# Performance work log

Hardware: AMD Instinct MI355X
Metric: run time of the kernel (lower is better)

## Reference

```python
import jax, jax.numpy as jnp
import numpy as np

B, S, D = 8, 2048, 512
MINF = 20000.0  # matches tf code's -20000.0 mask constant


def setup_inputs() -> dict:
    key = jax.random.key(0)
    k1, k2, k3 = jax.random.split(key, 3)
    x1 = jax.random.normal(k1, (B, S, D), dtype=jnp.float32)
    x2 = jax.random.normal(k2, (B, S, D), dtype=jnp.float32)
    # glorot_normal init for the learned (S, S) positional kernel
    std = np.sqrt(2.0 / (S + S)).astype(np.float32)
    kernel = jax.random.normal(k3, (S, S), dtype=jnp.float32) * std
    return {"x1": x1, "x2": x2, "kernel": kernel}


def reference(x1, x2, kernel):
    S_ = kernel.shape[0]
    # tf.matmul(kernel, inputs[i]) broadcasts (S,S) @ (B,S,D) -> (B,S,D)
    h1 = jnp.einsum('st,btd->bsd', kernel, x1)
    h2 = jnp.einsum('st,btd->bsd', kernel, x2)
    # att_scores: (B, S, S)
    scores = jnp.einsum('bsd,btd->bst', h1, h2)
    d_k = jnp.asarray(S_, dtype=scores.dtype) ** 0.5
    # upper_m[i,j] = -20000 for j > i (strictly upper), else 0; added BEFORE scaling
    row = jnp.arange(S_)
    mask = jnp.where(row[None, :] > row[:, None], -MINF, 0.0).astype(scores.dtype)
    attn = jax.nn.softmax((scores + mask) / d_k, axis=-1)
    # note: output attends over h1 (not h2), as in the original code
    return jnp.einsum('bst,btd->bsd', attn, h1)
```

## Files before the change

kernel.cpp:

```cpp
#include <hip/hip_runtime.h>
#include <hip/hip_bf16.h>

#define S_DIM 2048
#define D_DIM 512
#define B_DIM 8
#define SCALE 0.02209708691207961f

typedef __hip_bfloat16 bf16;
typedef short bf16x8 __attribute__((ext_vector_type(8)));
typedef float f32x4 __attribute__((ext_vector_type(4)));

__device__ __forceinline__ unsigned short f2b(float f) {
  __hip_bfloat16 h = __float2bfloat16(f);
  return __builtin_bit_cast(unsigned short, h);
}

__device__ __forceinline__ void load_lds16(const void* g, void* l) {
  __builtin_amdgcn_global_load_lds((const __attribute__((address_space(1))) void*)g,
                                   (__attribute__((address_space(3))) void*)l, 16, 0, 0);
}

__global__ void convert_k(const float* __restrict__ in, bf16* __restrict__ out, int n8) {
  int i = blockIdx.x * blockDim.x + threadIdx.x;
  if (i >= n8) return;
  const float4* p = (const float4*)in;
  float4 a = p[2 * i], b = p[2 * i + 1];
  bf16x8 r;
  r[0] = f2b(a.x); r[1] = f2b(a.y); r[2] = f2b(a.z); r[3] = f2b(a.w);
  r[4] = f2b(b.x); r[5] = f2b(b.y); r[6] = f2b(b.z); r[7] = f2b(b.w);
  ((bf16x8*)out)[i] = r;
}

__global__ void transpose_f2b(const float* __restrict__ in, bf16* __restrict__ out) {
  __shared__ float tile[32][33];
  int b = blockIdx.z;
  int c0 = blockIdx.x * 32;
  int r0 = blockIdx.y * 32;
  const float* ib = in + (size_t)b * S_DIM * D_DIM;
  bf16* ob = out + (size_t)b * S_DIM * D_DIM;
  int lr = threadIdx.x >> 5, lc = threadIdx.x & 31;
#pragma unroll
  for (int i = 0; i < 4; i++)
    tile[lr + i * 8][lc] = ib[(size_t)(r0 + lr + i * 8) * D_DIM + c0 + lc];
  __syncthreads();
#pragma unroll
  for (int i = 0; i < 4; i++) {
    int cc = lr + i * 8;
    ob[(size_t)(c0 + cc) * S_DIM + r0 + lc] = __float2bfloat16(tile[lc][cc]);
  }
}

__global__ void transpose_b2b(const bf16* __restrict__ in, bf16* __restrict__ out) {
  __shared__ bf16 tile[32][33];
  int b = blockIdx.z;
  int c0 = blockIdx.x * 32;
  int r0 = blockIdx.y * 32;
  const bf16* ib = in + (size_t)b * S_DIM * D_DIM;
  bf16* ob = out + (size_t)b * S_DIM * D_DIM;
  int lr = threadIdx.x >> 5, lc = threadIdx.x & 31;
#pragma unroll
  for (int i = 0; i < 4; i++)
    tile[lr + i * 8][lc] = ib[(size_t)(r0 + lr + i * 8) * D_DIM + c0 + lc];
  __syncthreads();
#pragma unroll
  for (int i = 0; i < 4; i++) {
    int cc = lr + i * 8;
    ob[(size_t)(c0 + cc) * S_DIM + r0 + lc] = tile[lc][cc];
  }
}

__global__ __launch_bounds__(256, 2) void gemm_bt(
    const bf16* __restrict__ A,
    const bf16* __restrict__ B1, const bf16* __restrict__ B2,
    bf16* __restrict__ C1, bf16* __restrict__ C2) {
  const int N = D_DIM, K = S_DIM;
  __shared__ bf16 As[128][32];
  __shared__ bf16 Bs[128][32];
  int z = blockIdx.z;
  int b = z & 7, which = z >> 3;
  const bf16* Bb = (which ? B2 : B1) + (size_t)b * D_DIM * S_DIM;
  bf16* Cb = (which ? C2 : C1) + (size_t)b * S_DIM * D_DIM;
  int m0 = blockIdx.y * 128, n0 = blockIdx.x * 128;
  int tid = threadIdx.x, wave = tid >> 6, lane = tid & 63;
  int wr = wave >> 1, wc = wave & 1;
  int srow = lane >> 2;
  int skh = (lane & 3) * 8;
  int lr16 = lane & 15, lk = (lane >> 4) * 8;
  f32x4 acc[4][4];
#pragma unroll
  for (int m = 0; m < 4; m++)
#pragma unroll
    for (int n = 0; n < 4; n++) acc[m][n] = (f32x4){0, 0, 0, 0};

  for (int k0 = 0; k0 < K; k0 += 32) {
#pragma unroll
    for (int c = 0; c < 2; c++) {
      int chunk = wave * 2 + c;
      int row = chunk * 16 + srow;
      load_lds16(A + (size_t)(m0 + row) * K + k0 + skh, (char*)&As[0][0] + chunk * 1024);
      load_lds16(Bb + (size_t)(n0 + row) * K + k0 + skh, (char*)&Bs[0][0] + chunk * 1024);
    }
    __syncthreads();
    bf16x8 af[4], bfr[4];
#pragma unroll
    for (int m = 0; m < 4; m++) af[m] = *(const bf16x8*)&As[wr * 64 + m * 16 + lr16][lk];
#pragma unroll
    for (int n = 0; n < 4; n++) bfr[n] = *(const bf16x8*)&Bs[wc * 64 + n * 16 + lr16][lk];
#pragma unroll
    for (int m = 0; m < 4; m++)
#pragma unroll
      for (int n = 0; n < 4; n++)
        acc[m][n] = __builtin_amdgcn_mfma_f32_16x16x32_bf16(af[m], bfr[n], acc[m][n], 0, 0, 0);
    __syncthreads();
  }
#pragma unroll
  for (int m = 0; m < 4; m++) {
    int grow0 = m0 + wr * 64 + m * 16 + (lane >> 4) * 4;
#pragma unroll
    for (int n = 0; n < 4; n++) {
      int gcol = n0 + wc * 64 + n * 16 + lr16;
#pragma unroll
      for (int r = 0; r < 4; r++)
        Cb[(size_t)(grow0 + r) * N + gcol] = __float2bfloat16(acc[m][n][r]);
    }
  }
}

__global__ __launch_bounds__(256, 2) void gemm_score(
    const bf16* __restrict__ H1, const bf16* __restrict__ H2,
    bf16* __restrict__ E, float* __restrict__ rowsum) {
  const int K = D_DIM;
  __shared__ bf16 As[128][32];
  __shared__ bf16 Bs[128][32];
  int pid = blockIdx.x;
  int b = pid & 7, tri = pid >> 3;
  int mt = (int)((sqrtf(8.0f * (float)tri + 1.0f) - 1.0f) * 0.5f);
  while ((mt + 1) * (mt + 2) / 2 <= tri) mt++;
  while (mt * (mt + 1) / 2 > tri) mt--;
  int nt = tri - mt * (mt + 1) / 2;
  const bf16* Ab = H1 + (size_t)b * S_DIM * D_DIM;
  const bf16* Bb = H2 + (size_t)b * S_DIM * D_DIM;
  bf16* Eb = E + (size_t)b * S_DIM * S_DIM;
  float* rs = rowsum + b * S_DIM;
  int m0 = mt * 128, n0 = nt * 128;
  int tid = threadIdx.x, wave = tid >> 6, lane = tid & 63;
  int wr = wave >> 1, wc = wave & 1;
  int srow = lane >> 2;
  int skh = (lane & 3) * 8;
  int l15 = lane & 15, lhi = lane >> 4;
  int lk = lhi * 8;
  f32x4 acc[4][4];
#pragma unroll
  for (int m = 0; m < 4; m++)
#pragma unroll
    for (int n = 0; n < 4; n++) acc[m][n] = (f32x4){0, 0, 0, 0};

  for (int k0 = 0; k0 < K; k0 += 32) {
#pragma unroll
    for (int c = 0; c < 2; c++) {
      int chunk = wave * 2 + c;
      int row = chunk * 16 + srow;
      load_lds16(Ab + (size_t)(m0 + row) * K + k0 + skh, (char*)&As[0][0] + chunk * 1024);
      load_lds16(Bb + (size_t)(n0 + row) * K + k0 + skh, (char*)&Bs[0][0] + chunk * 1024);
    }
    __syncthreads();
    bf16x8 af[4], bfr[4];
#pragma unroll
    for (int m = 0; m < 4; m++) af[m] = *(const bf16x8*)&As[wr * 64 + m * 16 + l15][lk];
#pragma unroll
    for (int n = 0; n < 4; n++) bfr[n] = *(const bf16x8*)&Bs[wc * 64 + n * 16 + l15][lk];
#pragma unroll
    for (int m = 0; m < 4; m++)
#pragma unroll
      for (int n = 0; n < 4; n++)
        acc[m][n] = __builtin_amdgcn_mfma_f32_16x16x32_bf16(af[m], bfr[n], acc[m][n], 0, 0, 0);
    __syncthreads();
  }
  float rp[4][4];
#pragma unroll
  for (int m = 0; m < 4; m++)
#pragma unroll
    for (int r = 0; r < 4; r++) rp[m][r] = 0.0f;
#pragma unroll
  for (int m = 0; m < 4; m++) {
#pragma unroll
    for (int n = 0; n < 4; n++) {
      int tg = n0 + wc * 64 + n * 16 + l15;
#pragma unroll
      for (int r = 0; r < 4; r++) {
        int sg = m0 + wr * 64 + m * 16 + lhi * 4 + r;
        float v = 0.0f;
        if (tg <= sg) v = __expf(acc[m][n][r] * SCALE);
        bf16 bv = __float2bfloat16(v);
        Eb[(size_t)sg * S_DIM + tg] = bv;
        rp[m][r] += __bfloat162float(bv);
      }
    }
  }
#pragma unroll
  for (int m = 0; m < 4; m++) {
#pragma unroll
    for (int r = 0; r < 4; r++) {
      float v = rp[m][r];
#pragma unroll
      for (int off = 1; off < 16; off <<= 1) v += __shfl_xor(v, off);
      if (l15 == 0) {
        int sg = m0 + wr * 64 + m * 16 + lhi * 4 + r;
        atomicAdd(rs + sg, v);
      }
    }
  }
}

__global__ __launch_bounds__(256, 2) void gemm_pv(
    const bf16* __restrict__ E, const bf16* __restrict__ H1T,
    const float* __restrict__ rowsum, float* __restrict__ out) {
  __shared__ bf16 As[128][32];
  __shared__ bf16 Bs[128][32];
  int pid = blockIdx.x;
  int b = pid & 7;
  int r_ = pid >> 3;
  int nt = r_ & 3;
  int mb = r_ >> 2;
  int mt = (mb < 8) ? 2 * mb : 31 - 2 * mb;
  int m0 = mt * 128, n0 = nt * 128;
  int KMAX = (mt + 1) * 128;
  const bf16* Ab = E + (size_t)b * S_DIM * S_DIM;
  const bf16* Bb = H1T + (size_t)b * D_DIM * S_DIM;
  const float* rs = rowsum + b * S_DIM;
  float* Cb = out + (size_t)b * S_DIM * D_DIM;
  int tid = threadIdx.x, wave = tid >> 6, lane = tid & 63;
  int wr = wave >> 1, wc = wave & 1;
  int srow = lane >> 2;
  int skh = (lane & 3) * 8;
  int l15 = lane & 15, lhi = lane >> 4;
  int lk = lhi * 8;
  f32x4 acc[4][4];
#pragma unroll
  for (int m = 0; m < 4; m++)
#pragma unroll
    for (int n = 0; n < 4; n++) acc[m][n] = (f32x4){0, 0, 0, 0};

  for (int k0 = 0; k0 < KMAX; k0 += 32) {
#pragma unroll
    for (int c = 0; c < 2; c++) {
      int chunk = wave * 2 + c;
      int row = chunk * 16 + srow;
      load_lds16(Ab + (size_t)(m0 + row) * S_DIM + k0 + skh, (char*)&As[0][0] + chunk * 1024);
      load_lds16(Bb + (size_t)(n0 + row) * S_DIM + k0 + skh, (char*)&Bs[0][0] + chunk * 1024);
    }
    __syncthreads();
    bf16x8 af[4], bfr[4];
#pragma unroll
    for (int m = 0; m < 4; m++) af[m] = *(const bf16x8*)&As[wr * 64 + m * 16 + l15][lk];
#pragma unroll
    for (int n = 0; n < 4; n++) bfr[n] = *(const bf16x8*)&Bs[wc * 64 + n * 16 + l15][lk];
#pragma unroll
    for (int m = 0; m < 4; m++)
#pragma unroll
      for (int n = 0; n < 4; n++)
        acc[m][n] = __builtin_amdgcn_mfma_f32_16x16x32_bf16(af[m], bfr[n], acc[m][n], 0, 0, 0);
    __syncthreads();
  }
#pragma unroll
  for (int m = 0; m < 4; m++) {
#pragma unroll
    for (int r = 0; r < 4; r++) {
      int sg = m0 + wr * 64 + m * 16 + lhi * 4 + r;
      float inv = 1.0f / rs[sg];
#pragma unroll
      for (int n = 0; n < 4; n++) {
        int gcol = n0 + wc * 64 + n * 16 + l15;
        Cb[(size_t)sg * D_DIM + gcol] = acc[m][n][r] * inv;
      }
    }
  }
}

extern "C" void kernel_launch(void* const* d_in, const int* in_sizes, int n_in,
                              void* d_out, int out_size, void* d_ws, size_t ws_size,
                              hipStream_t stream) {
  const float* x1 = (const float*)d_in[0];
  const float* x2 = (const float*)d_in[1];
  const float* km = (const float*)d_in[2];
  float* out = (float*)d_out;
  char* ws = (char*)d_ws;
  bf16* E    = (bf16*)(ws);
  bf16* Kbf  = (bf16*)(ws);
  bf16* x1t  = (bf16*)(ws + (8ull << 20));
  bf16* x2t  = (bf16*)(ws + (24ull << 20));
  bf16* h1n  = (bf16*)(ws + (64ull << 20));
  bf16* h2n  = (bf16*)(ws + (80ull << 20));
  bf16* h1t  = (bf16*)(ws + (96ull << 20));
  float* rowsum = (float*)(ws + (112ull << 20));

  convert_k<<<2048, 256, 0, stream>>>(km, Kbf, (S_DIM * S_DIM) / 8);
  transpose_f2b<<<dim3(16, 64, 8), 256, 0, stream>>>(x1, x1t);
  transpose_f2b<<<dim3(16, 64, 8), 256, 0, stream>>>(x2, x2t);
  gemm_bt<<<dim3(4, 16, 16), 256, 0, stream>>>(Kbf, x1t, x2t, h1n, h2n);
  transpose_b2b<<<dim3(16, 64, 8), 256, 0, stream>>>(h1n, h1t);
  hipMemsetAsync(rowsum, 0, B_DIM * S_DIM * sizeof(float), stream);
  gemm_score<<<136 * 8, 256, 0, stream>>>(h1n, h2n, E, rowsum);
  gemm_pv<<<512, 256, 0, stream>>>(E, h1t, rowsum, out);
}
```

Baseline: 197.2 us.

## Replace projection GEMM with triple-buffered, swizzled 256x128 tile kernel

Replaces the simple single-buffered gemm_bt projection GEMM with gemm_h. It uses 512-thread blocks on 256x128 output tiles and a K step of 64. A three-stage ring of LDS buffers is filled by asynchronous global-to-LDS loads, throttled with explicit vmcnt waits, so global loads overlap MFMA work. XOR-swizzled LDS addressing avoids bank conflicts, and s_setprio is raised around the MFMA burst. The x1/x2 work items are addressed as one contiguous 16-item batch through adjacent workspace regions. The cost is 144 KB of dynamic LDS per block, which limits occupancy, and the code depends on that exact workspace layout.

```diff
diff --git a/kernel.cpp b/kernel.cpp
--- a/kernel.cpp
+++ b/kernel.cpp
@@ -69,59 +69,109 @@
   }
 }
 
-__global__ __launch_bounds__(256, 2) void gemm_bt(
-    const bf16* __restrict__ A,
-    const bf16* __restrict__ B1, const bf16* __restrict__ B2,
-    bf16* __restrict__ C1, bf16* __restrict__ C2) {
-  const int N = D_DIM, K = S_DIM;
-  __shared__ bf16 As[128][32];
-  __shared__ bf16 Bs[128][32];
-  int z = blockIdx.z;
-  int b = z & 7, which = z >> 3;
-  const bf16* Bb = (which ? B2 : B1) + (size_t)b * D_DIM * S_DIM;
-  bf16* Cb = (which ? C2 : C1) + (size_t)b * S_DIM * D_DIM;
-  int m0 = blockIdx.y * 128, n0 = blockIdx.x * 128;
-  int tid = threadIdx.x, wave = tid >> 6, lane = tid & 63;
-  int wr = wave >> 1, wc = wave & 1;
-  int srow = lane >> 2;
-  int skh = (lane & 3) * 8;
-  int lr16 = lane & 15, lk = (lane >> 4) * 8;
+__global__ __launch_bounds__(512, 2) void gemm_h(
+    const bf16* __restrict__ A, const bf16* __restrict__ X, bf16* __restrict__ H) {
+  extern __shared__ char smem[];
+  const int pid = blockIdx.x;
+  const int item = pid & 15;
+  const int tt = pid >> 4;
+  const int mt = tt >> 2, ntl = tt & 3;
+  const int m0 = mt * 256, n0 = ntl * 128;
+  const bf16* Xi = X + (size_t)item * (D_DIM * S_DIM);
+  bf16* Hi = H + (size_t)item * (S_DIM * D_DIM);
+
+  const int tid = threadIdx.x;
+  const int w = tid >> 6, L = tid & 63;
+  const int l15 = L & 15, lhi = L >> 4;
+  const int wr = w >> 1, wc = w & 1;
+  const int lr8 = L >> 3;
+  const int sslot = ((L & 7) ^ lr8) * 8;
+
+  const bf16* paA[4];
+  const bf16* paB[2];
+#pragma unroll
+  for (int ld = 0; ld < 4; ld++)
+    paA[ld] = A + (size_t)(m0 + 32 * w + 8 * ld + lr8) * 2048 + sslot;
+#pragma unroll
+  for (int ld = 0; ld < 2; ld++)
+    paB[ld] = Xi + (size_t)(n0 + 16 * w + 8 * ld + lr8) * 2048 + sslot;
+
+  char* rA0 = smem;
+  char* rA1 = smem + 32768;
+  char* rA2 = smem + 65536;
+  char* rB0 = smem + 98304;
+  char* rB1 = smem + 98304 + 16384;
+  char* rB2 = smem + 98304 + 32768;
+
+  auto stage = [&](int t2, char* dA, char* dB) {
+#pragma unroll
+    for (int ld = 0; ld < 4; ld++)
+      load_lds16(paA[ld] + t2 * 64, dA + ((w * 4 + ld) << 10));
+#pragma unroll
+    for (int ld = 0; ld < 2; ld++)
+      load_lds16(paB[ld] + t2 * 64, dB + ((w * 2 + ld) << 10));
+  };
+
+  int offA[2][4], offB[2][4];
+#pragma unroll
+  for (int kk = 0; kk < 2; kk++) {
+#pragma unroll
+    for (int m = 0; m < 4; m++)
+      offA[kk][m] = (wr * 64 + m * 16 + l15) * 128 + ((((kk << 2) + lhi) ^ (L & 7)) << 4);
+#pragma unroll
+    for (int n = 0; n < 4; n++)
+      offB[kk][n] = (wc * 64 + n * 16 + l15) * 128 + ((((kk << 2) + lhi) ^ (L & 7)) << 4);
+  }
+
   f32x4 acc[4][4];
 #pragma unroll
   for (int m = 0; m < 4; m++)
 #pragma unroll
     for (int n = 0; n < 4; n++) acc[m][n] = (f32x4){0, 0, 0, 0};
 
-  for (int k0 = 0; k0 < K; k0 += 32) {
-#pragma unroll
-    for (int c = 0; c < 2; c++) {
-      int chunk = wave * 2 + c;
-      int row = chunk * 16 + srow;
-      load_lds16(A + (size_t)(m0 + row) * K + k0 + skh, (char*)&As[0][0] + chunk * 1024);
-      load_lds16(Bb + (size_t)(n0 + row) * K + k0 + skh, (char*)&Bs[0][0] + chunk * 1024);
-    }
-    __syncthreads();
-    bf16x8 af[4], bfr[4];
-#pragma unroll
-    for (int m = 0; m < 4; m++) af[m] = *(const bf16x8*)&As[wr * 64 + m * 16 + lr16][lk];
-#pragma unroll
-    for (int n = 0; n < 4; n++) bfr[n] = *(const bf16x8*)&Bs[wc * 64 + n * 16 + lr16][lk];
-#pragma unroll
-    for (int m = 0; m < 4; m++)
-#pragma unroll
-      for (int n = 0; n < 4; n++)
-        acc[m][n] = __builtin_amdgcn_mfma_f32_16x16x32_bf16(af[m], bfr[n], acc[m][n], 0, 0, 0);
-    __syncthreads();
-  }
+  stage(0, rA0, rB0);
+  stage(1, rA1, rB1);
+
+#pragma unroll 1
+  for (int t = 0; t < 32; ++t) {
+    if (t < 31) asm volatile("s_waitcnt vmcnt(6)" ::: "memory");
+    else        asm volatile("s_waitcnt vmcnt(0)" ::: "memory");
+    __builtin_amdgcn_s_barrier();
+    asm volatile("" ::: "memory");
+    if (t < 30) stage(t + 2, rA2, rB2);
+
+    bf16x8 af[2][4], bfr[2][4];
+#pragma unroll
+    for (int kk = 0; kk < 2; kk++) {
+#pragma unroll
+      for (int m = 0; m < 4; m++) af[kk][m] = *(const bf16x8*)(rA0 + offA[kk][m]);
+#pragma unroll
+      for (int n = 0; n < 4; n++) bfr[kk][n] = *(const bf16x8*)(rB0 + offB[kk][n]);
+    }
+    __builtin_amdgcn_s_setprio(1);
+#pragma unroll
+    for (int kk = 0; kk < 2; kk++)
+#pragma unroll
+      for (int m = 0; m < 4; m++)
+#pragma unroll
+        for (int n = 0; n < 4; n++)
+          acc[m][n] = __builtin_amdgcn_mfma_f32_16x16x32_bf16(af[kk][m], bfr[kk][n], acc[m][n], 0, 0, 0);
+    __builtin_amdgcn_s_setprio(0);
+
+    char* tA = rA0; rA0 = rA1; rA1 = rA2; rA2 = tA;
+    char* tB = rB0; rB0 = rB1; rB1 = rB2; rB2 = tB;
+  }
+
 #pragma unroll
   for (int m = 0; m < 4; m++) {
-    int grow0 = m0 + wr * 64 + m * 16 + (lane >> 4) * 4;
 #pragma unroll
     for (int n = 0; n < 4; n++) {
-      int gcol = n0 + wc * 64 + n * 16 + lr16;
-#pragma unroll
-      for (int r = 0; r < 4; r++)
-        Cb[(size_t)(grow0 + r) * N + gcol] = __float2bfloat16(acc[m][n][r]);
+      int col = n0 + wc * 64 + n * 16 + l15;
+#pragma unroll
+      for (int r = 0; r < 4; r++) {
+        int row = m0 + wr * 64 + m * 16 + lhi * 4 + r;
+        Hi[(size_t)row * D_DIM + col] = __float2bfloat16(acc[m][n][r]);
+      }
     }
   }
 }
@@ -288,16 +338,15 @@
   bf16* E    = (bf16*)(ws);
   bf16* Kbf  = (bf16*)(ws);
   bf16* x1t  = (bf16*)(ws + (8ull << 20));
-  bf16* x2t  = (bf16*)(ws + (24ull << 20));
   bf16* h1n  = (bf16*)(ws + (64ull << 20));
-  bf16* h2n  = (bf16*)(ws + (80ull << 20));
   bf16* h1t  = (bf16*)(ws + (96ull << 20));
   float* rowsum = (float*)(ws + (112ull << 20));
+  bf16* h2n  = (bf16*)(ws + (80ull << 20));
 
   convert_k<<<2048, 256, 0, stream>>>(km, Kbf, (S_DIM * S_DIM) / 8);
   transpose_f2b<<<dim3(16, 64, 8), 256, 0, stream>>>(x1, x1t);
-  transpose_f2b<<<dim3(16, 64, 8), 256, 0, stream>>>(x2, x2t);
-  gemm_bt<<<dim3(4, 16, 16), 256, 0, stream>>>(Kbf, x1t, x2t, h1n, h2n);
+  transpose_f2b<<<dim3(16, 64, 8), 256, 0, stream>>>(x2, (bf16*)(ws + (24ull << 20)));
+  gemm_h<<<512, 512, 147456, stream>>>(Kbf, x1t, h1n);
   transpose_b2b<<<dim3(16, 64, 8), 256, 0, stream>>>(h1n, h1t);
   hipMemsetAsync(rowsum, 0, B_DIM * S_DIM * sizeof(float), stream);
   gemm_score<<<136 * 8, 256, 0, stream>>>(h1n, h2n, E, rowsum);
```

After: 190.5 us. -3.4%, faster.

## Use 256x256 tiles with triple-buffered LDS pipeline for projection and score GEMMs

Applied to the files above, without the earlier changes.

Replaces the 128x128 projection and score GEMMs with 512-thread kernels computing 256x256 tiles. They stage operands through a three-buffer LDS ring with XOR-swizzled slots, using explicit vmcnt waits and one barrier per k-step. MFMA operands are swapped so each lane holds four consecutive output columns, which allows packed 8-byte bf16 stores. The score kernel applies the causal mask only on diagonal tiles and reduces row sums with two shuffles. The projection kernel covers both inputs in one flattened grid. The cost is 96KB of dynamic LDS per block, fewer blocks overall, and more wasted work in the now-larger diagonal tiles.

```diff
diff --git a/kernel.cpp b/kernel.cpp
--- a/kernel.cpp
+++ b/kernel.cpp
@@ -13,6 +13,9 @@
 __device__ __forceinline__ unsigned short f2b(float f) {
   __hip_bfloat16 h = __float2bfloat16(f);
   return __builtin_bit_cast(unsigned short, h);
+}
+__device__ __forceinline__ float b2f(unsigned short s) {
+  return __bfloat162float(__builtin_bit_cast(__hip_bfloat16, s));
 }
 
 __device__ __forceinline__ void load_lds16(const void* g, void* l) {
@@ -69,146 +72,208 @@
   }
 }
 
-__global__ __launch_bounds__(256, 2) void gemm_bt(
-    const bf16* __restrict__ A,
-    const bf16* __restrict__ B1, const bf16* __restrict__ B2,
-    bf16* __restrict__ C1, bf16* __restrict__ C2) {
-  const int N = D_DIM, K = S_DIM;
-  __shared__ bf16 As[128][32];
-  __shared__ bf16 Bs[128][32];
-  int z = blockIdx.z;
-  int b = z & 7, which = z >> 3;
-  const bf16* Bb = (which ? B2 : B1) + (size_t)b * D_DIM * S_DIM;
-  bf16* Cb = (which ? C2 : C1) + (size_t)b * S_DIM * D_DIM;
-  int m0 = blockIdx.y * 128, n0 = blockIdx.x * 128;
-  int tid = threadIdx.x, wave = tid >> 6, lane = tid & 63;
-  int wr = wave >> 1, wc = wave & 1;
-  int srow = lane >> 2;
-  int skh = (lane & 3) * 8;
-  int lr16 = lane & 15, lk = (lane >> 4) * 8;
-  f32x4 acc[4][4];
-#pragma unroll
-  for (int m = 0; m < 4; m++)
+__global__ __launch_bounds__(512, 2) void gemm_h(
+    const bf16* __restrict__ A, const bf16* __restrict__ X, bf16* __restrict__ H) {
+  extern __shared__ char smem[];
+  const int pid = blockIdx.x;
+  const int mt = pid & 7;
+  const int r_ = pid >> 3;
+  const int ntile = r_ & 1;
+  const int item = r_ >> 1;
+  const int m0 = mt * 256, n0 = ntile * 256;
+  const bf16* Xi = X + (size_t)item * (D_DIM * S_DIM);
+  bf16* Hi = H + (size_t)item * (S_DIM * D_DIM);
+
+  const int tid = threadIdx.x;
+  const int w = tid >> 6, L = tid & 63;
+  const int l15 = L & 15, lhi = L >> 4;
+  const int wr = w >> 2, wn = w & 3;
+
+  const int srow = tid >> 2;
+  const int sslot = ((tid & 3) ^ ((tid >> 3) & 3)) * 8;
+  const bf16* pA[2];
+  const bf16* pB[2];
+#pragma unroll
+  for (int ld = 0; ld < 2; ld++) {
+    pA[ld] = A + (size_t)(m0 + ld * 128 + srow) * 2048 + sslot;
+    pB[ld] = Xi + (size_t)(n0 + ld * 128 + srow) * 2048 + sslot;
+  }
+
+  char* A0 = smem;          char* A1 = smem + 16384;  char* A2 = smem + 32768;
+  char* B0 = smem + 49152;  char* B1 = smem + 65536;  char* B2 = smem + 81920;
+
+  auto stage = [&](int t2, char* dA, char* dB) {
+#pragma unroll
+    for (int ld = 0; ld < 2; ld++)
+      load_lds16(pA[ld] + t2 * 32, dA + ld * 8192 + w * 1024);
+#pragma unroll
+    for (int ld = 0; ld < 2; ld++)
+      load_lds16(pB[ld] + t2 * 32, dB + ld * 8192 + w * 1024);
+  };
+
+  const int xo = (lhi ^ ((l15 >> 1) & 3)) << 4;
+  int offA[8], offB[4];
+#pragma unroll
+  for (int m = 0; m < 8; m++) offA[m] = (wr * 128 + m * 16 + l15) * 64 + xo;
+#pragma unroll
+  for (int n = 0; n < 4; n++) offB[n] = (wn * 64 + n * 16 + l15) * 64 + xo;
+
+  f32x4 acc[8][4];
+#pragma unroll
+  for (int m = 0; m < 8; m++)
 #pragma unroll
     for (int n = 0; n < 4; n++) acc[m][n] = (f32x4){0, 0, 0, 0};
 
-  for (int k0 = 0; k0 < K; k0 += 32) {
-#pragma unroll
-    for (int c = 0; c < 2; c++) {
-      int chunk = wave * 2 + c;
-      int row = chunk * 16 + srow;
-      load_lds16(A + (size_t)(m0 + row) * K + k0 + skh, (char*)&As[0][0] + chunk * 1024);
-      load_lds16(Bb + (size_t)(n0 + row) * K + k0 + skh, (char*)&Bs[0][0] + chunk * 1024);
+  stage(0, A0, B0);
+  stage(1, A1, B1);
+
+#pragma unroll 1
+  for (int t = 0; t < 64; ++t) {
+    if (t < 63) asm volatile("s_waitcnt vmcnt(4)" ::: "memory");
+    else        asm volatile("s_waitcnt vmcnt(0)" ::: "memory");
+    __builtin_amdgcn_s_barrier();
+    asm volatile("" ::: "memory");
+    if (t < 62) stage(t + 2, A2, B2);
+
+    bf16x8 af[8], bfv[4];
+#pragma unroll
+    for (int m = 0; m < 8; m++) af[m] = *(const bf16x8*)(A0 + offA[m]);
+#pragma unroll
+    for (int n = 0; n < 4; n++) bfv[n] = *(const bf16x8*)(B0 + offB[n]);
+    __builtin_amdgcn_s_setprio(1);
+#pragma unroll
+    for (int m = 0; m < 8; m++)
+#pragma unroll
+      for (int n = 0; n < 4; n++)
+        acc[m][n] = __builtin_amdgcn_mfma_f32_16x16x32_bf16(bfv[n], af[m], acc[m][n], 0, 0, 0);
+    __builtin_amdgcn_s_setprio(0);
+
+    char* tA = A0; A0 = A1; A1 = A2; A2 = tA;
+    char* tB = B0; B0 = B1; B1 = B2; B2 = tB;
+  }
+
+#pragma unroll
+  for (int m = 0; m < 8; m++) {
+    int grow = m0 + wr * 128 + m * 16 + l15;
+#pragma unroll
+    for (int n = 0; n < 4; n++) {
+      int gcol = n0 + wn * 64 + n * 16 + lhi * 4;
+      uint2 u;
+      u.x = ((unsigned)f2b(acc[m][n][1]) << 16) | f2b(acc[m][n][0]);
+      u.y = ((unsigned)f2b(acc[m][n][3]) << 16) | f2b(acc[m][n][2]);
+      *(uint2*)(Hi + (size_t)grow * D_DIM + gcol) = u;
     }
-    __syncthreads();
-    bf16x8 af[4], bfr[4];
-#pragma unroll
-    for (int m = 0; m < 4; m++) af[m] = *(const bf16x8*)&As[wr * 64 + m * 16 + lr16][lk];
-#pragma unroll
-    for (int n = 0; n < 4; n++) bfr[n] = *(const bf16x8*)&Bs[wc * 64 + n * 16 + lr16][lk];
-#pragma unroll
-    for (int m = 0; m < 4; m++)
-#pragma unroll
-      for (int n = 0; n < 4; n++)
-        acc[m][n] = __builtin_amdgcn_mfma_f32_16x16x32_bf16(af[m], bfr[n], acc[m][n], 0, 0, 0);
-    __syncthreads();
-  }
-#pragma unroll
-  for (int m = 0; m < 4; m++) {
-    int grow0 = m0 + wr * 64 + m * 16 + (lane >> 4) * 4;
-#pragma unroll
-    for (int n = 0; n < 4; n++) {
-      int gcol = n0 + wc * 64 + n * 16 + lr16;
-#pragma unroll
-      for (int r = 0; r < 4; r++)
-        Cb[(size_t)(grow0 + r) * N + gcol] = __float2bfloat16(acc[m][n][r]);
-    }
-  }
-}
-
-__global__ __launch_bounds__(256, 2) void gemm_score(
+  }
+}
+
+__global__ __launch_bounds__(512, 2) void gemm_score(
     const bf16* __restrict__ H1, const bf16* __restrict__ H2,
     bf16* __restrict__ E, float* __restrict__ rowsum) {
-  const int K = D_DIM;
-  __shared__ bf16 As[128][32];
-  __shared__ bf16 Bs[128][32];
-  int pid = blockIdx.x;
-  int b = pid & 7, tri = pid >> 3;
+  extern __shared__ char smem[];
+  const int pid = blockIdx.x;
+  const int b = pid & 7;
+  const int tri = pid >> 3;
   int mt = (int)((sqrtf(8.0f * (float)tri + 1.0f) - 1.0f) * 0.5f);
   while ((mt + 1) * (mt + 2) / 2 <= tri) mt++;
   while (mt * (mt + 1) / 2 > tri) mt--;
-  int nt = tri - mt * (mt + 1) / 2;
+  const int nt = tri - mt * (mt + 1) / 2;
+  const int m0 = mt * 256, n0 = nt * 256;
+  const bool diag = (mt == nt);
   const bf16* Ab = H1 + (size_t)b * S_DIM * D_DIM;
   const bf16* Bb = H2 + (size_t)b * S_DIM * D_DIM;
   bf16* Eb = E + (size_t)b * S_DIM * S_DIM;
   float* rs = rowsum + b * S_DIM;
-  int m0 = mt * 128, n0 = nt * 128;
-  int tid = threadIdx.x, wave = tid >> 6, lane = tid & 63;
-  int wr = wave >> 1, wc = wave & 1;
-  int srow = lane >> 2;
-  int skh = (lane & 3) * 8;
-  int l15 = lane & 15, lhi = lane >> 4;
-  int lk = lhi * 8;
-  f32x4 acc[4][4];
-#pragma unroll
-  for (int m = 0; m < 4; m++)
+
+  const int tid = threadIdx.x;
+  const int w = tid >> 6, L = tid & 63;
+  const int l15 = L & 15, lhi = L >> 4;
+  const int wr = w >> 2, wn = w & 3;
+
+  const int srow = tid >> 2;
+  const int sslot = ((tid & 3) ^ ((tid >> 3) & 3)) * 8;
+  const bf16* pA[2];
+  const bf16* pB[2];
+#pragma unroll
+  for (int ld = 0; ld < 2; ld++) {
+    pA[ld] = Ab + (size_t)(m0 + ld * 128 + srow) * D_DIM + sslot;
+    pB[ld] = Bb + (size_t)(n0 + ld * 128 + srow) * D_DIM + sslot;
+  }
+
+  char* A0 = smem;          char* A1 = smem + 16384;  char* A2 = smem + 32768;
+  char* B0 = smem + 49152;  char* B1 = smem + 65536;  char* B2 = smem + 81920;
+
+  auto stage = [&](int t2, char* dA, char* dB) {
+#pragma unroll
+    for (int ld = 0; ld < 2; ld++)
+      load_lds16(pA[ld] + t2 * 32, dA + ld * 8192 + w * 1024);
+#pragma unroll
+    for (int ld = 0; ld < 2; ld++)
+      load_lds16(pB[ld] + t2 * 32, dB + ld * 8192 + w * 1024);
+  };
+
+  const int xo = (lhi ^ ((l15 >> 1) & 3)) << 4;
+  int offA[8], offB[4];
+#pragma unroll
+  for (int m = 0; m < 8; m++) offA[m] = (wr * 128 + m * 16 + l15) * 64 + xo;
+#pragma unroll
+  for (int n = 0; n < 4; n++) offB[n] = (wn * 64 + n * 16 + l15) * 64 + xo;
+
+  f32x4 acc[8][4];
+#pragma unroll
+  for (int m = 0; m < 8; m++)
 #pragma unroll
     for (int n = 0; n < 4; n++) acc[m][n] = (f32x4){0, 0, 0, 0};
 
-  for (int k0 = 0; k0 < K; k0 += 32) {
-#pragma unroll
-    for (int c = 0; c < 2; c++) {
-      int chunk = wave * 2 + c;
-      int row = chunk * 16 + srow;
-      load_lds16(Ab + (size_t)(m0 + row) * K + k0 + skh, (char*)&As[0][0] + chunk * 1024);
-      load_lds16(Bb + (size_t)(n0 + row) * K + k0 + skh, (char*)&Bs[0][0] + chunk * 1024);
+  stage(0, A0, B0);
+  stage(1, A1, B1);
+
+#pragma unroll 1
+  for (int t = 0; t < 16; ++t) {
+    if (t < 15) asm volatile("s_waitcnt vmcnt(4)" ::: "memory");
+    else        asm volatile("s_waitcnt vmcnt(0)" ::: "memory");
+    __builtin_amdgcn_s_barrier();
+    asm volatile("" ::: "memory");
+    if (t < 14) stage(t + 2, A2, B2);
+
+    bf16x8 af[8], bfv[4];
+#pragma unroll
+    for (int m = 0; m < 8; m++) af[m] = *(const bf16x8*)(A0 + offA[m]);
+#pragma unroll
+    for (int n = 0; n < 4; n++) bfv[n] = *(const bf16x8*)(B0 + offB[n]);
+    __builtin_amdgcn_s_setprio(1);
+#pragma unroll
+    for (int m = 0; m < 8; m++)
+#pragma unroll
+      for (int n = 0; n < 4; n++)
+        acc[m][n] = __builtin_amdgcn_mfma_f32_16x16x32_bf16(bfv[n], af[m], acc[m][n], 0, 0, 0);
+    __builtin_amdgcn_s_setprio(0);
+
+    char* tA = A0; A0 = A1; A1 = A2; A2 = tA;
+    char* tB = B0; B0 = B1; B1 = B2; B2 = tB;
+  }
+
+#pragma unroll
+  for (int m = 0; m < 8; m++) {
+    int sg = m0 + wr * 128 + m * 16 + l15;
+    float rp = 0.0f;
+#pragma unroll
+    for (int n = 0; n < 4; n++) {
+      int tg0 = n0 + wn * 64 + n * 16 + lhi * 4;
+      unsigned short e[4];
+#pragma unroll
+      for (int r = 0; r < 4; r++) {
+        float v = (!diag || (tg0 + r) <= sg) ? __expf(acc[m][n][r] * SCALE) : 0.0f;
+        e[r] = f2b(v);
+        rp += b2f(e[r]);
+      }
+      uint2 u;
+      u.x = ((unsigned)e[1] << 16) | e[0];
+      u.y = ((unsigned)e[3] << 16) | e[2];
+      *(uint2*)(Eb + (size_t)sg * S_DIM + tg0) = u;
     }
-    __syncthreads();
-    bf16x8 af[4], bfr[4];
-#pragma unroll
-    for (int m = 0; m < 4; m++) af[m] = *(const bf16x8*)&As[wr * 64 + m * 16 + l15][lk];
-#pragma unroll
-    for (int n = 0; n < 4; n++) bfr[n] = *(const bf16x8*)&Bs[wc * 64 + n * 16 + l15][lk];
-#pragma unroll
-    for (int m = 0; m < 4; m++)
-#pragma unroll
-      for (int n = 0; n < 4; n++)
-        acc[m][n] = __builtin_amdgcn_mfma_f32_16x16x32_bf16(af[m], bfr[n], acc[m][n], 0, 0, 0);
-    __syncthreads();
-  }
-  float rp[4][4];
-#pragma unroll
-  for (int m = 0; m < 4; m++)
-#pragma unroll
-    for (int r = 0; r < 4; r++) rp[m][r] = 0.0f;
-#pragma unroll
-  for (int m = 0; m < 4; m++) {
-#pragma unroll
-    for (int n = 0; n < 4; n++) {
-      int tg = n0 + wc * 64 + n * 16 + l15;
-#pragma unroll
-      for (int r = 0; r < 4; r++) {
-        int sg = m0 + wr * 64 + m * 16 + lhi * 4 + r;
-        float v = 0.0f;
-        if (tg <= sg) v = __expf(acc[m][n][r] * SCALE);
-        bf16 bv = __float2bfloat16(v);
-        Eb[(size_t)sg * S_DIM + tg] = bv;
-        rp[m][r] += __bfloat162float(bv);
-      }
-    }
-  }
-#pragma unroll
-  for (int m = 0; m < 4; m++) {
-#pragma unroll
-    for (int r = 0; r < 4; r++) {
-      float v = rp[m][r];
-#pragma unroll
-      for (int off = 1; off < 16; off <<= 1) v += __shfl_xor(v, off);
-      if (l15 == 0) {
-        int sg = m0 + wr * 64 + m * 16 + lhi * 4 + r;
-        atomicAdd(rs + sg, v);
-      }
-    }
+    rp += __shfl_xor(rp, 16);
+    rp += __shfl_xor(rp, 32);
+    if (lhi == 0) atomicAdd(rs + sg, rp);
   }
 }
 
@@ -297,9 +362,9 @@
   convert_k<<<2048, 256, 0, stream>>>(km, Kbf, (S_DIM * S_DIM) / 8);
   transpose_f2b<<<dim3(16, 64, 8), 256, 0, stream>>>(x1, x1t);
   transpose_f2b<<<dim3(16, 64, 8), 256, 0, stream>>>(x2, x2t);
-  gemm_bt<<<dim3(4, 16, 16), 256, 0, stream>>>(Kbf, x1t, x2t, h1n, h2n);
+  gemm_h<<<256, 512, 98304, stream>>>(Kbf, x1t, h1n);
   transpose_b2b<<<dim3(16, 64, 8), 256, 0, stream>>>(h1n, h1t);
   hipMemsetAsync(rowsum, 0, B_DIM * S_DIM * sizeof(float), stream);
-  gemm_score<<<136 * 8, 256, 0, stream>>>(h1n, h2n, E, rowsum);
+  gemm_score<<<288, 512, 98304, stream>>>(h1n, h2n, E, rowsum);
   gemm_pv<<<512, 256, 0, stream>>>(E, h1t, rowsum, out);
 }
```

After: 190.8 us. 1.03x faster.
